# Performance work log

Measured on AMD Instinct MI355X. Metric: run time of the kernel, lower is better.

The kernel has to match this reference:

```python
import jax, jax.numpy as jnp
import numpy as np

S, H, NUM_TAG, D_LEN, MAX_LEN = 256, 1024, 20, 10, 1000


def setup_inputs() -> dict:
    key = jax.random.key(0)
    ks = jax.random.split(key, 6)
    sc = lambda d: 1.0 / np.sqrt(d)
    return {
        "hidden": jax.random.normal(ks[0], (S, H), jnp.float32),
        "target": jax.random.randint(ks[1], (S,), 0, NUM_TAG),
        "attn_w1": jax.random.normal(ks[2], (H, H), jnp.float32) * sc(H),
        "attn_b1": jnp.zeros((H,), jnp.float32),
        "attn_w2": jax.random.normal(ks[3], (H, 1), jnp.float32) * sc(H),
        "attn_b2": jnp.zeros((1,), jnp.float32),
        "len_emb": jax.random.normal(ks[4], (MAX_LEN, D_LEN), jnp.float32),
        "fc_w": jax.random.normal(ks[5], (3 * H + D_LEN, NUM_TAG), jnp.float32) * sc(3 * H + D_LEN),
        "fc_b": jnp.zeros((NUM_TAG,), jnp.float32),
    }


def reference(hidden, target, attn_w1, attn_b1, attn_w2, attn_b2, len_emb, fc_w, fc_b):
    S_, H_ = hidden.shape
    # attention scores [S]
    a = (jnp.tanh(hidden @ attn_w1 + attn_b1) @ attn_w2 + attn_b2)[:, 0]
    # prefix sums for contiguous-window softmax pooling
    e = jnp.exp(a - jnp.max(a))                                   # [S]
    Zc = jnp.concatenate([jnp.zeros((1,), e.dtype), jnp.cumsum(e)])                      # [S+1]
    Pc = jnp.concatenate([jnp.zeros((1, H_), e.dtype), jnp.cumsum(e[:, None] * hidden, axis=0)])  # [S+1,H]
    ii, jj = jnp.triu_indices(S_, k=1)                            # all spans i<j, loop order
    span = (Pc[jj + 1] - Pc[ii]) / (Zc[jj + 1] - Zc[ii])[:, None]  # softmax-weighted pooling
    lemb = len_emb[jj - ii + 1]                                   # segment length embedding (no grad in torch)
    feats = jnp.concatenate([span, hidden[ii], hidden[jj], lemb], axis=-1)  # [P, 3H+10]
    logits = feats @ fc_w + fc_b                                  # [P, num_tag]
    # is_span labels via run ids
    change = jnp.concatenate([jnp.array([True]), target[1:] != target[:-1]])
    run_id = jnp.cumsum(change.astype(jnp.int32))
    start = change
    end = jnp.concatenate([target[:-1] != target[1:], jnp.array([True])])
    labels = jnp.where((run_id[ii] == run_id[jj]) & start[ii] & end[jj], target[jj], 0)
    logp = jax.nn.log_softmax(logits, axis=-1)
    loss = -jnp.mean(jnp.take_along_axis(logp, labels[:, None].astype(jnp.int32), axis=1))
    return logits, loss.reshape(1)
```

## Files before the change

kernel.cpp:

```cpp
#include <hip/hip_runtime.h>
#include <math.h>

#define S 256
#define H 1024
#define NPAIR 32640

#define WS_T     0
#define WS_HP    2097152
#define WS_A     2220032
#define WS_ZC    2220544
#define WS_HW0   2220804
#define WS_HW1   2225924
#define WS_HW2   2231044
#define WS_PW    2236164
#define WS_LW    2241304
#define WS_LOSSP 2246444
#define WS_RUN   2246700
#define WS_START 2246956
#define WS_END   2247212

__device__ __forceinline__ float tanh_fast(float x) {
    const float xc = fminf(fmaxf(x, -15.f), 15.f);
    const float ex = __expf(2.f * xc);
    return (ex - 1.f) / (ex + 1.f);
}

__global__ __launch_bounds__(256) void K1(const float* __restrict__ hidden,
                                          const float* __restrict__ w1,
                                          const float* __restrict__ fcw,
                                          float* __restrict__ ws) {
    const int tid = threadIdx.x;
    const int b = blockIdx.x;

    if (b < 512) {
        __shared__ __align__(16) float shH[128][4];
        const int kc = b >> 6, rg = b & 63;
        #pragma unroll
        for (int e = 0; e < 2; e++) {
            const int li = e * 256 + tid;
            const int kk = li & 127, r = li >> 7;
            shH[kk][r] = hidden[(rg * 4 + r) * H + kc * 128 + kk];
        }
        __syncthreads();
        float4 a0 = make_float4(0.f, 0.f, 0.f, 0.f), a1 = a0, a2 = a0, a3 = a0;
        const float* wp = w1 + (size_t)(kc * 128) * H + tid * 4;
        #pragma unroll 8
        for (int k = 0; k < 128; k++) {
            const float4 wv = *(const float4*)&wp[(size_t)k * H];
            const float4 h4 = *(const float4*)&shH[k][0];
            a0.x = fmaf(h4.x, wv.x, a0.x); a0.y = fmaf(h4.x, wv.y, a0.y);
            a0.z = fmaf(h4.x, wv.z, a0.z); a0.w = fmaf(h4.x, wv.w, a0.w);
            a1.x = fmaf(h4.y, wv.x, a1.x); a1.y = fmaf(h4.y, wv.y, a1.y);
            a1.z = fmaf(h4.y, wv.z, a1.z); a1.w = fmaf(h4.y, wv.w, a1.w);
            a2.x = fmaf(h4.z, wv.x, a2.x); a2.y = fmaf(h4.z, wv.y, a2.y);
            a2.z = fmaf(h4.z, wv.z, a2.z); a2.w = fmaf(h4.z, wv.w, a2.w);
            a3.x = fmaf(h4.w, wv.x, a3.x); a3.y = fmaf(h4.w, wv.y, a3.y);
            a3.z = fmaf(h4.w, wv.z, a3.z); a3.w = fmaf(h4.w, wv.w, a3.w);
        }
        float* op = ws + WS_T + (size_t)kc * (S * H) + (size_t)(rg * 4) * H + tid * 4;
        *(float4*)&op[0]     = a0;
        *(float4*)&op[H]     = a1;
        *(float4*)&op[2 * H] = a2;
        *(float4*)&op[3 * H] = a3;
    } else {
        __shared__ __align__(16) float shHT[128][20];
        const int hb = b - 512;
        const int rg = hb & 15, kc = hb >> 4;
        {
            const int c = tid & 127, rr = tid >> 7;
            #pragma unroll
            for (int e = 0; e < 8; e++) {
                const int r = e * 2 + rr;
                shHT[c][r] = hidden[(rg * 16 + r) * H + kc * 128 + c];
            }
        }
        __syncthreads();
        if (tid < 240) {
            const int t = tid % 20, g = tid / 20;
            const int p = g >> 2, rsub = g & 3;
            const float* fw = fcw + (size_t)(p * H + kc * 128) * 20 + t;
            float a0 = 0.f, a1 = 0.f, a2 = 0.f, a3 = 0.f;
            #pragma unroll 8
            for (int k = 0; k < 128; k++) {
                const float w = fw[k * 20];
                const float4 h4 = *(const float4*)&shHT[k][rsub * 4];
                a0 = fmaf(h4.x, w, a0);
                a1 = fmaf(h4.y, w, a1);
                a2 = fmaf(h4.z, w, a2);
                a3 = fmaf(h4.w, w, a3);
            }
            float* hpo = ws + WS_HP + ((size_t)(kc * 3 + p) * 256 + rg * 16 + rsub * 4) * 20 + t;
            hpo[0] = a0; hpo[20] = a1; hpo[40] = a2; hpo[60] = a3;
        }
    }
}

__global__ __launch_bounds__(256) void K2(const float* __restrict__ b1,
                                          const float* __restrict__ w2,
                                          float* __restrict__ ws) {
    const int b = blockIdx.x, tid = threadIdx.x;
    __shared__ float sred[256];
    {
        const int c = tid * 4;
        float4 sum = make_float4(0.f, 0.f, 0.f, 0.f);
        #pragma unroll
        for (int kcz = 0; kcz < 8; kcz++) {
            const float4 tv = *(const float4*)&ws[WS_T + (size_t)kcz * (S * H) + (size_t)b * H + c];
            sum.x += tv.x; sum.y += tv.y; sum.z += tv.z; sum.w += tv.w;
        }
        const float4 b4 = *(const float4*)&b1[c];
        const float4 w4 = *(const float4*)&w2[c];
        sred[tid] = tanh_fast(sum.x + b4.x) * w4.x
                  + tanh_fast(sum.y + b4.y) * w4.y
                  + tanh_fast(sum.z + b4.z) * w4.z
                  + tanh_fast(sum.w + b4.w) * w4.w;
    }
    __syncthreads();
    for (int off = 128; off > 0; off >>= 1) {
        if (tid < off) sred[tid] += sred[tid + off];
        __syncthreads();
    }
    if (tid == 0) ws[WS_A + b] = sred[0];

    if (tid < 60) {
        const int t = tid % 20, p = tid / 20;
        float s = 0.f;
        #pragma unroll
        for (int kc = 0; kc < 8; kc++)
            s += ws[WS_HP + ((size_t)(kc * 3 + p) * 256 + b) * 20 + t];
        const int base = (p == 0) ? WS_HW0 : (p == 1) ? WS_HW1 : WS_HW2;
        ws[base + b * 20 + t] = s;
    }
}

__global__ __launch_bounds__(256) void K3(const float* __restrict__ b2,
                                          const int* __restrict__ target,
                                          const float* __restrict__ lenemb,
                                          const float* __restrict__ fcw,
                                          float* __restrict__ ws) {
    const int s = threadIdx.x;
    __shared__ float shf[256], she[256];
    __shared__ int shi[256], shtg[256];
    __shared__ float shlen[2550];
    __shared__ float shfct[200];
    __shared__ float shw0[5120];
    __shared__ float shpw[5120];
    __shared__ float soff[4][20];

    for (int idx = s; idx < 2550; idx += 256) shlen[idx] = lenemb[20 + idx];
    if (s < 200) shfct[s] = fcw[61440 + s];
    for (int idx = s; idx < 5120; idx += 256) shw0[idx] = ws[WS_HW0 + idx];

    shtg[s] = target[s];
    const float a = ws[WS_A + s] + b2[0];
    shf[s] = a;
    __syncthreads();

    for (int item = s; item < 5100; item += 256) {
        const int L2i = item / 20, t = item % 20;
        float v = 0.f;
        #pragma unroll
        for (int d = 0; d < 10; d++)
            v = fmaf(shlen[L2i * 10 + d], shfct[d * 20 + t], v);
        ws[WS_LW + (L2i + 2) * 20 + t] = v;
    }

    for (int off = 128; off > 0; off >>= 1) {
        if (s < off) shf[s] = fmaxf(shf[s], shf[s + off]);
        __syncthreads();
    }
    const float mx = shf[0];
    __syncthreads();
    const float ev = __expf(a - mx);
    she[s] = ev;
    shf[s] = ev;
    const int chg = (s == 0) ? 1 : (shtg[s] != shtg[s - 1]);
    shi[s] = chg;
    __syncthreads();
    for (int off = 1; off < 256; off <<= 1) {
        const float fv = (s >= off) ? shf[s - off] : 0.f;
        const int   iv = (s >= off) ? shi[s - off] : 0;
        __syncthreads();
        shf[s] += fv;
        shi[s] += iv;
        __syncthreads();
    }
    ws[WS_ZC + s + 1] = shf[s];
    if (s == 0) ws[WS_ZC] = 0.f;
    ((int*)ws)[WS_RUN + s]   = shi[s];
    ((int*)ws)[WS_START + s] = chg;
    ((int*)ws)[WS_END + s]   = (s == 255) ? 1 : (shtg[s] != shtg[s + 1]);

    if (s < 80) {
        const int t = s % 20, seg = s / 20;
        const int base = seg * 64;
        float pw = 0.f;
        for (int k = 0; k < 64; k++) {
            pw = fmaf(she[base + k], shw0[(base + k) * 20 + t], pw);
            shpw[(base + k) * 20 + t] = pw;
        }
    }
    __syncthreads();
    if (s < 20) {
        const float T0 = shpw[63 * 20 + s], T1 = shpw[127 * 20 + s], T2 = shpw[191 * 20 + s];
        soff[0][s] = 0.f; soff[1][s] = T0; soff[2][s] = T0 + T1; soff[3][s] = T0 + T1 + T2;
    }
    __syncthreads();
    for (int item = s; item < 5140; item += 256) {
        const int r = item / 20, t = item % 20;
        const float v = (r == 0) ? 0.f : shpw[(r - 1) * 20 + t] + soff[(r - 1) >> 6][t];
        ws[WS_PW + item] = v;
    }
}

__global__ __launch_bounds__(256) void K4(const int* __restrict__ target,
                                          const float* __restrict__ fcb,
                                          float* __restrict__ out,
                                          float* __restrict__ ws) {
    const int tid = threadIdx.x;
    const int p = blockIdx.x * 256 + tid;
    __shared__ float sred[256];
    float lossacc = 0.f;
    if (p < NPAIR) {
        int i = (int)((511.0f - sqrtf((float)(261121 - 8 * p))) * 0.5f);
        while ((i + 1) * (510 - i) <= 2 * p) ++i;
        while (i > 0 && i * (511 - i) > 2 * p) --i;
        const int j = p - i * (511 - i) / 2 + i + 1;

        const float Zci  = ws[WS_ZC + i];
        const float invz = 1.f / (ws[WS_ZC + j + 1] - Zci);
        const int L = j - i + 1;
        const int* runid = (const int*)ws + WS_RUN;
        const int* stA   = (const int*)ws + WS_START;
        const int* enA   = (const int*)ws + WS_END;
        const int lbl = (runid[i] == runid[j] && stA[i] && enA[j]) ? target[j] : 0;

        const float4* pwj4 = (const float4*)(ws + WS_PW + (j + 1) * 20);
        const float4* pwi4 = (const float4*)(ws + WS_PW + i * 20);
        const float4* h14  = (const float4*)(ws + WS_HW1 + i * 20);
        const float4* h24  = (const float4*)(ws + WS_HW2 + j * 20);
        const float4* lw4  = (const float4*)(ws + WS_LW + L * 20);
        const float4* fb4  = (const float4*)fcb;
        float4* op4 = (float4*)(out + (size_t)p * 20);

        float lg[20];
        float mx = -1e30f, chosen = 0.f;
        #pragma unroll
        for (int q = 0; q < 5; q++) {
            const float4 aj = pwj4[q], ai = pwi4[q];
            const float4 bi = h14[q],  bj = h24[q];
            const float4 cl = lw4[q],  fb = fb4[q];
            float4 r;
            r.x = (aj.x - ai.x) * invz + bi.x + bj.x + cl.x + fb.x;
            r.y = (aj.y - ai.y) * invz + bi.y + bj.y + cl.y + fb.y;
            r.z = (aj.z - ai.z) * invz + bi.z + bj.z + cl.z + fb.z;
            r.w = (aj.w - ai.w) * invz + bi.w + bj.w + cl.w + fb.w;
            op4[q] = r;
            lg[q * 4 + 0] = r.x; lg[q * 4 + 1] = r.y;
            lg[q * 4 + 2] = r.z; lg[q * 4 + 3] = r.w;
            mx = fmaxf(mx, fmaxf(fmaxf(r.x, r.y), fmaxf(r.z, r.w)));
            chosen = (q * 4 + 0 == lbl) ? r.x : chosen;
            chosen = (q * 4 + 1 == lbl) ? r.y : chosen;
            chosen = (q * 4 + 2 == lbl) ? r.z : chosen;
            chosen = (q * 4 + 3 == lbl) ? r.w : chosen;
        }
        float se = 0.f;
        #pragma unroll
        for (int t = 0; t < 20; t++) se += __expf(lg[t] - mx);
        lossacc = -(chosen - mx - __logf(se));
    }
    sred[tid] = lossacc;
    __syncthreads();
    for (int off = 128; off > 0; off >>= 1) {
        if (tid < off) sred[tid] += sred[tid + off];
        __syncthreads();
    }
    if (tid == 0) ws[WS_LOSSP + blockIdx.x] = sred[0];
}

__global__ __launch_bounds__(128) void K5(float* __restrict__ out,
                                          float* __restrict__ ws) {
    __shared__ float sh[128];
    const int t = threadIdx.x;
    sh[t] = ws[WS_LOSSP + t];
    __syncthreads();
    for (int off = 64; off > 0; off >>= 1) {
        if (t < off) sh[t] += sh[t + off];
        __syncthreads();
    }
    if (t == 0) out[(size_t)NPAIR * 20] = sh[0] / (float)NPAIR;
}

extern "C" void kernel_launch(void* const* d_in, const int* in_sizes, int n_in,
                              void* d_out, int out_size, void* d_ws, size_t ws_size,
                              hipStream_t stream) {
    (void)in_sizes; (void)n_in; (void)out_size; (void)ws_size;
    const float* hidden = (const float*)d_in[0];
    const int*   target = (const int*)d_in[1];
    const float* w1     = (const float*)d_in[2];
    const float* b1     = (const float*)d_in[3];
    const float* w2     = (const float*)d_in[4];
    const float* b2     = (const float*)d_in[5];
    const float* lenemb = (const float*)d_in[6];
    const float* fcw    = (const float*)d_in[7];
    const float* fcb    = (const float*)d_in[8];
    float* out = (float*)d_out;
    float* ws  = (float*)d_ws;

    K1<<<640, 256, 0, stream>>>(hidden, w1, fcw, ws);
    K2<<<256, 256, 0, stream>>>(b1, w2, ws);
    K3<<<1, 256, 0, stream>>>(b2, target, lenemb, fcw, ws);
    K4<<<128, 256, 0, stream>>>(target, fcb, out, ws);
    K5<<<1, 128, 0, stream>>>(out, ws);
}
```

Measured before the change: 42.74 us.

## Fuse prefix-scan stage into pair-logits kernel with per-row redundant scans

Moves the length-embedding projection into K2 (block 0) and merges the single-block scan kernel into the pair-logits kernel. Each of 255 blocks now handles one start index i, recomputes the max/exp/prefix scans and the 20-wide weighted prefix in shared memory, then produces logits for all j>i. This drops one kernel launch and the workspace round-trips for Zc, PW and the label arrays, and removes the sqrt-based pair index decode. In exchange every block redoes the serial scan work and loads 20KB of HW0, and half the threads in late blocks sit idle.

```diff
diff --git a/kernel.cpp b/kernel.cpp
--- a/kernel.cpp
+++ b/kernel.cpp
@@ -8,16 +8,11 @@
 #define WS_T     0
 #define WS_HP    2097152
 #define WS_A     2220032
-#define WS_ZC    2220544
 #define WS_HW0   2220804
 #define WS_HW1   2225924
 #define WS_HW2   2231044
-#define WS_PW    2236164
 #define WS_LW    2241304
 #define WS_LOSSP 2246444
-#define WS_RUN   2246700
-#define WS_START 2246956
-#define WS_END   2247212
 
 __device__ __forceinline__ float tanh_fast(float x) {
     const float xc = fminf(fmaxf(x, -15.f), 15.f);
@@ -97,6 +92,8 @@
 
 __global__ __launch_bounds__(256) void K2(const float* __restrict__ b1,
                                           const float* __restrict__ w2,
+                                          const float* __restrict__ lenemb,
+                                          const float* __restrict__ fcw,
                                           float* __restrict__ ws) {
     const int b = blockIdx.x, tid = threadIdx.x;
     __shared__ float sred[256];
@@ -131,45 +128,45 @@
         const int base = (p == 0) ? WS_HW0 : (p == 1) ? WS_HW1 : WS_HW2;
         ws[base + b * 20 + t] = s;
     }
-}
-
-__global__ __launch_bounds__(256) void K3(const float* __restrict__ b2,
-                                          const int* __restrict__ target,
-                                          const float* __restrict__ lenemb,
-                                          const float* __restrict__ fcw,
-                                          float* __restrict__ ws) {
-    const int s = threadIdx.x;
+
+    if (b == 0) {
+        for (int item = tid; item < 5100; item += 256) {
+            const int L2i = item / 20, t = item % 20;
+            float v = 0.f;
+            #pragma unroll
+            for (int d = 0; d < 10; d++)
+                v = fmaf(lenemb[(L2i + 2) * 10 + d], fcw[(3072 + d) * 20 + t], v);
+            ws[WS_LW + (L2i + 2) * 20 + t] = v;
+        }
+    }
+}
+
+__global__ __launch_bounds__(256) void K3(const int* __restrict__ target,
+                                          const float* __restrict__ b2,
+                                          const float* __restrict__ fcb,
+                                          float* __restrict__ out,
+                                          float* __restrict__ ws) {
+    const int i = blockIdx.x;
+    const int j = threadIdx.x;
+    const int s = j;
     __shared__ float shf[256], she[256];
     __shared__ int shi[256], shtg[256];
-    __shared__ float shlen[2550];
-    __shared__ float shfct[200];
     __shared__ float shw0[5120];
     __shared__ float shpw[5120];
     __shared__ float soff[4][20];
-
-    for (int idx = s; idx < 2550; idx += 256) shlen[idx] = lenemb[20 + idx];
-    if (s < 200) shfct[s] = fcw[61440 + s];
+    __shared__ float sPwi[20], shw1i[20], sfcb[20];
+    __shared__ float sred[256];
+
     for (int idx = s; idx < 5120; idx += 256) shw0[idx] = ws[WS_HW0 + idx];
-
     shtg[s] = target[s];
     const float a = ws[WS_A + s] + b2[0];
-    shf[s] = a;
-    __syncthreads();
-
-    for (int item = s; item < 5100; item += 256) {
-        const int L2i = item / 20, t = item % 20;
-        float v = 0.f;
-        #pragma unroll
-        for (int d = 0; d < 10; d++)
-            v = fmaf(shlen[L2i * 10 + d], shfct[d * 20 + t], v);
-        ws[WS_LW + (L2i + 2) * 20 + t] = v;
-    }
-
-    for (int off = 128; off > 0; off >>= 1) {
-        if (s < off) shf[s] = fmaxf(shf[s], shf[s + off]);
-        __syncthreads();
-    }
-    const float mx = shf[0];
+    sred[s] = a;
+    __syncthreads();
+    for (int off = 128; off > 0; off >>= 1) {
+        if (s < off) sred[s] = fmaxf(sred[s], sred[s + off]);
+        __syncthreads();
+    }
+    const float mx = sred[0];
     __syncthreads();
     const float ev = __expf(a - mx);
     she[s] = ev;
@@ -185,12 +182,6 @@
         shi[s] += iv;
         __syncthreads();
     }
-    ws[WS_ZC + s + 1] = shf[s];
-    if (s == 0) ws[WS_ZC] = 0.f;
-    ((int*)ws)[WS_RUN + s]   = shi[s];
-    ((int*)ws)[WS_START + s] = chg;
-    ((int*)ws)[WS_END + s]   = (s == 255) ? 1 : (shtg[s] != shtg[s + 1]);
-
     if (s < 80) {
         const int t = s % 20, seg = s / 20;
         const int base = seg * 64;
@@ -204,61 +195,47 @@
     if (s < 20) {
         const float T0 = shpw[63 * 20 + s], T1 = shpw[127 * 20 + s], T2 = shpw[191 * 20 + s];
         soff[0][s] = 0.f; soff[1][s] = T0; soff[2][s] = T0 + T1; soff[3][s] = T0 + T1 + T2;
-    }
-    __syncthreads();
-    for (int item = s; item < 5140; item += 256) {
-        const int r = item / 20, t = item % 20;
-        const float v = (r == 0) ? 0.f : shpw[(r - 1) * 20 + t] + soff[(r - 1) >> 6][t];
-        ws[WS_PW + item] = v;
-    }
-}
-
-__global__ __launch_bounds__(256) void K4(const int* __restrict__ target,
-                                          const float* __restrict__ fcb,
-                                          float* __restrict__ out,
-                                          float* __restrict__ ws) {
-    const int tid = threadIdx.x;
-    const int p = blockIdx.x * 256 + tid;
-    __shared__ float sred[256];
+        sPwi[s]  = (i == 0) ? 0.f : shpw[(i - 1) * 20 + s] + soff[(i - 1) >> 6][s];
+        shw1i[s] = ws[WS_HW1 + i * 20 + s];
+        sfcb[s]  = fcb[s];
+    }
+    __syncthreads();
+
     float lossacc = 0.f;
-    if (p < NPAIR) {
-        int i = (int)((511.0f - sqrtf((float)(261121 - 8 * p))) * 0.5f);
-        while ((i + 1) * (510 - i) <= 2 * p) ++i;
-        while (i > 0 && i * (511 - i) > 2 * p) --i;
-        const int j = p - i * (511 - i) / 2 + i + 1;
-
-        const float Zci  = ws[WS_ZC + i];
-        const float invz = 1.f / (ws[WS_ZC + j + 1] - Zci);
+    if (j > i) {
+        const float ZCi  = (i == 0) ? 0.f : shf[i - 1];
+        const float invz = 1.f / (shf[j] - ZCi);
         const int L = j - i + 1;
-        const int* runid = (const int*)ws + WS_RUN;
-        const int* stA   = (const int*)ws + WS_START;
-        const int* enA   = (const int*)ws + WS_END;
-        const int lbl = (runid[i] == runid[j] && stA[i] && enA[j]) ? target[j] : 0;
-
-        const float4* pwj4 = (const float4*)(ws + WS_PW + (j + 1) * 20);
-        const float4* pwi4 = (const float4*)(ws + WS_PW + i * 20);
-        const float4* h14  = (const float4*)(ws + WS_HW1 + i * 20);
-        const float4* h24  = (const float4*)(ws + WS_HW2 + j * 20);
-        const float4* lw4  = (const float4*)(ws + WS_LW + L * 20);
-        const float4* fb4  = (const float4*)fcb;
+        const int sti = (i == 0) ? 1 : (shtg[i] != shtg[i - 1]);
+        const int enj = (j == 255) ? 1 : (shtg[j] != shtg[j + 1]);
+        const int lbl = (shi[i] == shi[j] && sti && enj) ? shtg[j] : 0;
+
+        const float4* pj4 = (const float4*)&shpw[j * 20];
+        const float4* so4 = (const float4*)&soff[j >> 6][0];
+        const float4* pi4 = (const float4*)sPwi;
+        const float4* h14 = (const float4*)shw1i;
+        const float4* h24 = (const float4*)&ws[WS_HW2 + j * 20];
+        const float4* lw4 = (const float4*)&ws[WS_LW + L * 20];
+        const float4* fb4 = (const float4*)sfcb;
+        const int p = i * (511 - i) / 2 + (j - i - 1);
         float4* op4 = (float4*)(out + (size_t)p * 20);
 
         float lg[20];
-        float mx = -1e30f, chosen = 0.f;
+        float mxl = -1e30f, chosen = 0.f;
         #pragma unroll
         for (int q = 0; q < 5; q++) {
-            const float4 aj = pwj4[q], ai = pwi4[q];
-            const float4 bi = h14[q],  bj = h24[q];
-            const float4 cl = lw4[q],  fb = fb4[q];
+            const float4 pj = pj4[q], so = so4[q], pi = pi4[q];
+            const float4 h1 = h14[q], h2 = h24[q];
+            const float4 lw = lw4[q], fb = fb4[q];
             float4 r;
-            r.x = (aj.x - ai.x) * invz + bi.x + bj.x + cl.x + fb.x;
-            r.y = (aj.y - ai.y) * invz + bi.y + bj.y + cl.y + fb.y;
-            r.z = (aj.z - ai.z) * invz + bi.z + bj.z + cl.z + fb.z;
-            r.w = (aj.w - ai.w) * invz + bi.w + bj.w + cl.w + fb.w;
+            r.x = (pj.x + so.x - pi.x) * invz + h1.x + h2.x + lw.x + fb.x;
+            r.y = (pj.y + so.y - pi.y) * invz + h1.y + h2.y + lw.y + fb.y;
+            r.z = (pj.z + so.z - pi.z) * invz + h1.z + h2.z + lw.z + fb.z;
+            r.w = (pj.w + so.w - pi.w) * invz + h1.w + h2.w + lw.w + fb.w;
             op4[q] = r;
             lg[q * 4 + 0] = r.x; lg[q * 4 + 1] = r.y;
             lg[q * 4 + 2] = r.z; lg[q * 4 + 3] = r.w;
-            mx = fmaxf(mx, fmaxf(fmaxf(r.x, r.y), fmaxf(r.z, r.w)));
+            mxl = fmaxf(mxl, fmaxf(fmaxf(r.x, r.y), fmaxf(r.z, r.w)));
             chosen = (q * 4 + 0 == lbl) ? r.x : chosen;
             chosen = (q * 4 + 1 == lbl) ? r.y : chosen;
             chosen = (q * 4 + 2 == lbl) ? r.z : chosen;
@@ -266,25 +243,25 @@
         }
         float se = 0.f;
         #pragma unroll
-        for (int t = 0; t < 20; t++) se += __expf(lg[t] - mx);
-        lossacc = -(chosen - mx - __logf(se));
-    }
-    sred[tid] = lossacc;
-    __syncthreads();
-    for (int off = 128; off > 0; off >>= 1) {
-        if (tid < off) sred[tid] += sred[tid + off];
-        __syncthreads();
-    }
-    if (tid == 0) ws[WS_LOSSP + blockIdx.x] = sred[0];
-}
-
-__global__ __launch_bounds__(128) void K5(float* __restrict__ out,
-                                          float* __restrict__ ws) {
-    __shared__ float sh[128];
+        for (int t = 0; t < 20; t++) se += __expf(lg[t] - mxl);
+        lossacc = -(chosen - mxl - __logf(se));
+    }
+    sred[j] = lossacc;
+    __syncthreads();
+    for (int off = 128; off > 0; off >>= 1) {
+        if (j < off) sred[j] += sred[j + off];
+        __syncthreads();
+    }
+    if (j == 0) ws[WS_LOSSP + i] = sred[0];
+}
+
+__global__ __launch_bounds__(256) void K4(float* __restrict__ out,
+                                          float* __restrict__ ws) {
+    __shared__ float sh[256];
     const int t = threadIdx.x;
-    sh[t] = ws[WS_LOSSP + t];
-    __syncthreads();
-    for (int off = 64; off > 0; off >>= 1) {
+    sh[t] = (t < 255) ? ws[WS_LOSSP + t] : 0.f;
+    __syncthreads();
+    for (int off = 128; off > 0; off >>= 1) {
         if (t < off) sh[t] += sh[t + off];
         __syncthreads();
     }
@@ -308,8 +285,7 @@
     float* ws  = (float*)d_ws;
 
     K1<<<640, 256, 0, stream>>>(hidden, w1, fcw, ws);
-    K2<<<256, 256, 0, stream>>>(b1, w2, ws);
-    K3<<<1, 256, 0, stream>>>(b2, target, lenemb, fcw, ws);
-    K4<<<128, 256, 0, stream>>>(target, fcb, out, ws);
-    K5<<<1, 128, 0, stream>>>(out, ws);
-}
+    K2<<<256, 256, 0, stream>>>(b1, w2, lenemb, fcw, ws);
+    K3<<<255, 256, 0, stream>>>(target, b2, fcb, out, ws);
+    K4<<<1, 256, 0, stream>>>(out, ws);
+}
```

After: 37.20 us (median of 3 runs). 1.15x faster.
